# Optimization experiments

Hardware: AMD Instinct MI355X
Metric: run time of the kernel (lower is better)

Reference implementation:

```python
import jax, jax.numpy as jnp
import numpy as np
from jax import lax

EPS = 1e-5

def binarize(x):
    # sign forward, straight-through (identity) backward, matching torch .data-trick Binarize
    return x + lax.stop_gradient(jnp.sign(x) - x)

def conv2d(x, w, pad):
    return lax.conv_general_dilated(x, w, window_strides=(1, 1),
                                    padding=[(pad, pad), (pad, pad)],
                                    dimension_numbers=('NCHW', 'OIHW', 'NCHW'))

def maxpool_k2s1(x):
    return lax.reduce_window(x, -jnp.inf, lax.max, (1, 1, 2, 2), (1, 1, 1, 1), 'VALID')

def batchnorm(x, g, b):
    # training-mode BN: batch statistics over (N, H, W)
    mean = jnp.mean(x, axis=(0, 2, 3), keepdims=True)
    var = jnp.var(x, axis=(0, 2, 3), keepdims=True)
    return (x - mean) * lax.rsqrt(var + EPS) * g[None, :, None, None] + b[None, :, None, None]

def hardtanh(x):
    return jnp.clip(x, -1.0, 1.0)

def setup_inputs() -> dict:
    key = jax.random.key(0)
    ks = jax.random.split(key, 11)
    B = 4096
    return {
        'x':   jax.random.normal(ks[0], (B, 12, 12, 15), jnp.float32),
        'w1':  jax.random.normal(ks[1], (48, 12, 3, 3), jnp.float32) * 0.1,
        'g1':  1.0 + 0.1 * jax.random.normal(ks[2], (48,), jnp.float32),
        'b1':  0.1 * jax.random.normal(ks[3], (48,), jnp.float32),
        'w2':  jax.random.normal(ks[4], (48, 48, 3, 3), jnp.float32) * 0.1,
        'g2':  1.0 + 0.1 * jax.random.normal(ks[5], (48,), jnp.float32),
        'b2':  0.1 * jax.random.normal(ks[6], (48,), jnp.float32),
        'w3':  jax.random.normal(ks[7], (48, 48, 3, 3), jnp.float32) * 0.1,
        'g3':  1.0 + 0.1 * jax.random.normal(ks[8], (48,), jnp.float32),
        'b3':  0.1 * jax.random.normal(ks[9], (48,), jnp.float32),
        'wfc': jax.random.normal(ks[10], (5, 54 * 48), jnp.float32) * 0.02,
    }

def reference(x, w1, g1, b1, w2, g2, b2, w3, g3, b3, wfc):
    # BinarizeConv2d binarizes activations (in_channels != 3) and weights; returns binarized input too
    xb1 = binarize(x)                                  # [B,12,12,15]
    h = conv2d(xb1, binarize(w1), pad=1)               # [B,48,12,15]
    h = maxpool_k2s1(h)                                # [B,48,11,14]
    h = hardtanh(batchnorm(h, g1, b1))
    xb2 = binarize(h)
    h = conv2d(xb2, binarize(w2), pad=0)               # [B,48,9,12]
    h = hardtanh(batchnorm(h, g2, b2))
    xb3 = binarize(h)
    h = conv2d(xb3, binarize(w3), pad=0)               # [B,48,7,10]
    h = maxpool_k2s1(h)                                # [B,48,6,9] -> 54 spatial
    h = hardtanh(batchnorm(h, g3, b3))
    f = h.reshape(h.shape[0], -1)                      # [B, 2592]
    fb = binarize(f)
    out = fb @ binarize(wfc).T                         # [B, 5]  (LogSoftmax defined but never applied)
    return (out, xb1, xb2, xb3, fb)
```

## Files before the change

### kernel.cpp

```cpp
#include <hip/hip_runtime.h>
#include <stdint.h>

typedef unsigned long long u64;
typedef unsigned short u16;

#define NB 4096

#define WS_STATS 0
#define WS_CONST 18432
#define WS_W1P   20480
#define WS_W2P   24576
#define WS_W3P   28672
#define WS_WFCP  32768
#define WS_A1    40960
#define WS_P1    5111808

#define OUT_OFF 0
#define XB1_OFF 20480
#define XB2_OFF 8867840
#define XB3_OFF 39145472
#define FB_OFF  60379136

__device__ __forceinline__ float fsign(float v) {
    return (v > 0.0f) ? 1.0f : ((v < 0.0f) ? -1.0f : 0.0f);
}

__global__ __launch_bounds__(512)
void kw_pack(const float* __restrict__ w1, const float* __restrict__ w2,
             const float* __restrict__ w3, const float* __restrict__ wfc,
             u16* __restrict__ W1P, u64* __restrict__ W2P, u64* __restrict__ W3P,
             u64* __restrict__ WFCP, long long* __restrict__ stats) {
    int t = threadIdx.x;
    for (int i = t; i < 2304; i += 512) stats[i] = 0;
    if (t < 432) {
        int oc = t / 9, p = t % 9;
        u16 m1 = 0;
        for (int c = 0; c < 12; ++c)
            if (w1[oc*108 + c*9 + p] > 0.0f) m1 |= (u16)(1u << c);
        W1P[t] = m1;
        u64 m2 = 0, m3 = 0;
        for (int c = 0; c < 48; ++c) {
            if (w2[oc*432 + c*9 + p] > 0.0f) m2 |= (1ull << c);
            if (w3[oc*432 + c*9 + p] > 0.0f) m3 |= (1ull << c);
        }
        W2P[t] = m2;
        W3P[t] = m3;
    }
    if (t < 205) {
        int o = t / 41, j = t % 41;
        u64 m = 0;
        for (int l = 0; l < 64; ++l) {
            int k = j*64 + l;
            if (k < 2592 && wfc[o*2592 + k] > 0.0f) m |= (1ull << l);
        }
        WFCP[t] = m;
    }
}

__global__ __launch_bounds__(64)
void kbn(const float* __restrict__ g, const float* __restrict__ bb,
         const long long* __restrict__ st, float* __restrict__ cst, float Nf) {
    int t = threadIdx.x;
    if (t < 48) {
        long long s = 0, q = 0;
        #pragma unroll
        for (int k = 0; k < 8; ++k) { s += st[t*8 + k]; q += st[(48 + t)*8 + k]; }
        double N = (double)Nf;
        double mean = (double)s / N;
        double var  = (double)q / N - mean*mean;
        double scale = (double)g[t] / sqrt(var + 1e-5);
        cst[t]      = (float)scale;
        cst[48 + t] = (float)((double)bb[t] - mean*scale);
    }
}

__global__ __launch_bounds__(256)
void k0_binx(const float* __restrict__ x, float* __restrict__ dout,
             u16* __restrict__ A1) {
    int id = blockIdx.x*256 + threadIdx.x;
    int b = id / 45, s4 = id % 45;
    const float4* xp = (const float4*)(x + b*2160);
    float4* op = (float4*)(dout + XB1_OFF + (size_t)b*2160);
    u16 m0 = 0, m1 = 0, m2 = 0, m3 = 0;
    #pragma unroll
    for (int c = 0; c < 12; ++c) {
        float4 v = xp[c*45 + s4];
        float4 o;
        o.x = fsign(v.x); o.y = fsign(v.y); o.z = fsign(v.z); o.w = fsign(v.w);
        op[c*45 + s4] = o;
        u16 bit = (u16)(1u << c);
        if (v.x > 0.0f) m0 |= bit;
        if (v.y > 0.0f) m1 |= bit;
        if (v.z > 0.0f) m2 |= bit;
        if (v.w > 0.0f) m3 |= bit;
    }
    ushort4 mm; mm.x = m0; mm.y = m1; mm.z = m2; mm.w = m3;
    *((ushort4*)(A1 + b*180 + s4*4)) = mm;
}

__global__ __launch_bounds__(192)
void k1_conv1(const u16* __restrict__ W1, const u16* __restrict__ A1,
              int* __restrict__ P1, u64* __restrict__ stats) {
    __shared__ u16 As[180];
    __shared__ int cmap_i[2160];
    __shared__ int pl_i[1848];
    signed char* cmap = (signed char*)cmap_i;
    signed char* pl = (signed char*)pl_i;
    int t = threadIdx.x, b = blockIdx.x;
    if (t < 180) As[t] = A1[b*180 + t];
    __syncthreads();
    if (t < 180) {
        int y = t / 15, xx = t % 15;
        u16 tap[9], msk[9];
        int nv = 0;
        #pragma unroll
        for (int ky = 0; ky < 3; ++ky) {
            #pragma unroll
            for (int kx = 0; kx < 3; ++kx) {
                int yy = y + ky - 1, xc = xx + kx - 1;
                bool v = (yy >= 0 && yy < 12 && xc >= 0 && xc < 15);
                int yl = min(max(yy, 0), 11), xl = min(max(xc, 0), 14);
                tap[ky*3+kx] = As[yl*15 + xl];
                msk[ky*3+kx] = v ? (u16)0xFFFF : (u16)0;
                nv += v ? 12 : 0;
            }
        }
        #pragma unroll 4
        for (int oc = 0; oc < 48; ++oc) {
            int acc = 0;
            #pragma unroll
            for (int k = 0; k < 9; ++k)
                acc += __popc((unsigned)((u16)(tap[k] ^ W1[oc*9 + k]) & msk[k]));
            cmap[oc*180 + t] = (signed char)(nv - 2*acc);
        }
    }
    __syncthreads();
    int* gp = P1 + (size_t)b*1848;
    for (int i4 = t; i4 < 1848; i4 += 192) {
        int r = 0;
        #pragma unroll
        for (int u = 0; u < 4; ++u) {
            int i = i4*4 + u;
            int c = i / 154, s = i % 154, py = s / 14, px = s % 14;
            int base = c*180 + py*15 + px;
            int mx = max(max((int)cmap[base],    (int)cmap[base+1]),
                         max((int)cmap[base+15], (int)cmap[base+16]));
            r |= (mx & 0xff) << (8*u);
        }
        pl_i[i4] = r;
        gp[i4] = r;
    }
    __syncthreads();
    int wv = t >> 6, ln = t & 63, slot = b & 7;
    for (int c = wv; c < 48; c += 3) {
        int sum = 0, sq = 0;
        for (int s = ln; s < 154; s += 64) {
            int v = pl[c*154 + s];
            sum += v; sq += v*v;
        }
        #pragma unroll
        for (int off = 32; off >= 1; off >>= 1) {
            sum += __shfl_down(sum, off);
            sq  += __shfl_down(sq, off);
        }
        if (ln == 0) {
            atomicAdd((u64*)&stats[c*8 + slot],        (u64)(long long)sum);
            atomicAdd((u64*)&stats[(48 + c)*8 + slot], (u64)(long long)sq);
        }
    }
}

__global__ __launch_bounds__(256)
void kA_bn1conv2(const float* __restrict__ cst, const int4* __restrict__ P1,
                 float* __restrict__ dout, u64* __restrict__ A2,
                 const u64* __restrict__ W2, u64* __restrict__ stats) {
    __shared__ float sc[48], sh[48];
    __shared__ int sm_i[1848];
    __shared__ u64 As[154];
    __shared__ short c2s[5184];
    signed char* sm = (signed char*)sm_i;
    int t = threadIdx.x, b = blockIdx.x;
    const int4* gp = P1 + (size_t)b*462;
    for (int i = t; i < 462; i += 256) ((int4*)sm_i)[i] = gp[i];
    if (t < 48) sc[t] = cst[t];
    else if (t < 96) sh[t - 48] = cst[t];
    __syncthreads();
    float4* xo = (float4*)(dout + XB2_OFF + (size_t)b*7392);
    for (int i4 = t; i4 < 1848; i4 += 256) {
        int pv = sm_i[i4];
        int i = i4*4;
        float4 o;
        int c0 = i/154, c1 = (i+1)/154, c2i = (i+2)/154, c3 = (i+3)/154;
        o.x = fsign(sc[c0]*(float)(signed char)(pv)        + sh[c0]);
        o.y = fsign(sc[c1]*(float)(signed char)(pv >> 8)   + sh[c1]);
        o.z = fsign(sc[c2i]*(float)(signed char)(pv >> 16) + sh[c2i]);
        o.w = fsign(sc[c3]*(float)(signed char)(pv >> 24)  + sh[c3]);
        xo[i4] = o;
    }
    if (t < 154) {
        u64 m = 0;
        #pragma unroll
        for (int c = 0; c < 48; ++c)
            if (sc[c]*(float)sm[c*154 + t] + sh[c] > 0.0f) m |= (1ull << c);
        As[t] = m;
        A2[(size_t)b*154 + t] = m;
    }
    __syncthreads();
    if (t < 216) {
        int pos = (t < 108) ? t : (t - 108);
        int ocb = (t < 108) ? 0 : 24;
        int oy = pos / 12, ox = pos % 12;
        u64 tap[9];
        #pragma unroll
        for (int ky = 0; ky < 3; ++ky)
            #pragma unroll
            for (int kx = 0; kx < 3; ++kx)
                tap[ky*3+kx] = As[(oy+ky)*14 + ox + kx];
        #pragma unroll 4
        for (int oc = ocb; oc < ocb + 24; ++oc) {
            int acc = 0;
            #pragma unroll
            for (int k = 0; k < 9; ++k)
                acc += __popcll(tap[k] ^ W2[oc*9 + k]);
            c2s[oc*108 + pos] = (short)(432 - 2*acc);
        }
    }
    __syncthreads();
    int wv = t >> 6, ln = t & 63, slot = b & 7;
    for (int c = wv; c < 48; c += 4) {
        int sum = 0, sq = 0;
        for (int s = ln; s < 108; s += 64) {
            int v = c2s[c*108 + s];
            sum += v; sq += v*v;
        }
        #pragma unroll
        for (int off = 32; off >= 1; off >>= 1) {
            sum += __shfl_down(sum, off);
            sq  += __shfl_down(sq, off);
        }
        if (ln == 0) {
            atomicAdd((u64*)&stats[(96 + c)*8 + slot],  (u64)(long long)sum);
            atomicAdd((u64*)&stats[(144 + c)*8 + slot], (u64)(long long)sq);
        }
    }
}

__global__ __launch_bounds__(256)
void kB_bn2conv3(const float* __restrict__ cst, const u64* __restrict__ A2,
                 const u64* __restrict__ W2, const u64* __restrict__ W3,
                 float* __restrict__ dout, short* __restrict__ P3,
                 u64* __restrict__ stats) {
    __shared__ float sc[48], sh[48];
    __shared__ u64 As[154];
    __shared__ short c2s[5184];
    __shared__ u64 A3[108];
    __shared__ short cm[3360];
    __shared__ short pls[2592];
    int t = threadIdx.x, b = blockIdx.x;
    if (t < 154) As[t] = A2[(size_t)b*154 + t];
    if (t < 48) sc[t] = cst[t];
    else if (t < 96) sh[t - 48] = cst[t];
    __syncthreads();
    if (t < 216) {
        int pos = (t < 108) ? t : (t - 108);
        int ocb = (t < 108) ? 0 : 24;
        int oy = pos / 12, ox = pos % 12;
        u64 tap[9];
        #pragma unroll
        for (int ky = 0; ky < 3; ++ky)
            #pragma unroll
            for (int kx = 0; kx < 3; ++kx)
                tap[ky*3+kx] = As[(oy+ky)*14 + ox + kx];
        #pragma unroll 4
        for (int oc = ocb; oc < ocb + 24; ++oc) {
            int acc = 0;
            #pragma unroll
            for (int k = 0; k < 9; ++k)
                acc += __popcll(tap[k] ^ W2[oc*9 + k]);
            c2s[oc*108 + pos] = (short)(432 - 2*acc);
        }
    }
    __syncthreads();
    float4* xo = (float4*)(dout + XB3_OFF + (size_t)b*5184);
    for (int i4 = t; i4 < 1296; i4 += 256) {
        int c = i4 / 27, s4 = i4 % 27;
        short4 v4 = *(const short4*)&c2s[c*108 + s4*4];
        float4 o;
        o.x = fsign(sc[c]*(float)v4.x + sh[c]);
        o.y = fsign(sc[c]*(float)v4.y + sh[c]);
        o.z = fsign(sc[c]*(float)v4.z + sh[c]);
        o.w = fsign(sc[c]*(float)v4.w + sh[c]);
        xo[i4] = o;
    }
    if (t < 108) {
        u64 m = 0;
        #pragma unroll
        for (int c = 0; c < 48; ++c)
            if (sc[c]*(float)c2s[c*108 + t] + sh[c] > 0.0f) m |= (1ull << c);
        A3[t] = m;
    }
    __syncthreads();
    if (t < 210) {
        int grp = (t < 70) ? 0 : ((t < 140) ? 1 : 2);
        int pos = t - grp*70;
        int ocb = grp*16;
        int oy = pos / 10, ox = pos % 10;
        u64 tap[9];
        #pragma unroll
        for (int ky = 0; ky < 3; ++ky)
            #pragma unroll
            for (int kx = 0; kx < 3; ++kx)
                tap[ky*3+kx] = A3[(oy+ky)*12 + ox + kx];
        #pragma unroll 4
        for (int oc = ocb; oc < ocb + 16; ++oc) {
            int acc = 0;
            #pragma unroll
            for (int k = 0; k < 9; ++k)
                acc += __popcll(tap[k] ^ W3[oc*9 + k]);
            cm[oc*70 + pos] = (short)(432 - 2*acc);
        }
    }
    __syncthreads();
    int* p3g = (int*)(P3 + (size_t)b*2592);
    for (int i2 = t; i2 < 1296; i2 += 256) {
        int i = i2*2;
        int c = i / 54, s = i % 54, py = s / 9, px = s % 9;
        int base = c*70 + py*10 + px;
        int m0 = max(max((int)cm[base],    (int)cm[base+1]),
                     max((int)cm[base+10], (int)cm[base+11]));
        int m1 = max(max((int)cm[base+1],  (int)cm[base+2]),
                     max((int)cm[base+11], (int)cm[base+12]));
        if (px == 8) {
            int base2 = c*70 + (py+1)*10;
            m1 = max(max((int)cm[base2],    (int)cm[base2+1]),
                     max((int)cm[base2+10], (int)cm[base2+11]));
        }
        pls[i] = (short)m0;
        pls[i+1] = (short)m1;
        p3g[i2] = (m0 & 0xffff) | (m1 << 16);
    }
    __syncthreads();
    int wv = t >> 6, ln = t & 63, slot = b & 7;
    for (int c = wv; c < 48; c += 4) {
        int sum = 0, sq = 0;
        if (ln < 54) {
            int v = pls[c*54 + ln];
            sum = v; sq = v*v;
        }
        #pragma unroll
        for (int off = 32; off >= 1; off >>= 1) {
            sum += __shfl_down(sum, off);
            sq  += __shfl_down(sq, off);
        }
        if (ln == 0) {
            atomicAdd((u64*)&stats[(192 + c)*8 + slot], (u64)(long long)sum);
            atomicAdd((u64*)&stats[(240 + c)*8 + slot], (u64)(long long)sq);
        }
    }
}

__global__ __launch_bounds__(256)
void kC_fbfc(const float* __restrict__ cst, const short* __restrict__ P3,
             const u64* __restrict__ WFC, float* __restrict__ dout) {
    __shared__ float sc[48], sh[48];
    __shared__ short4 sm4[648];
    __shared__ unsigned char nib[648];
    __shared__ u64 fbb[41];
    short* sm = (short*)sm4;
    int t = threadIdx.x, b = blockIdx.x;
    const short4* p3 = (const short4*)(P3 + (size_t)b*2592);
    for (int i4 = t; i4 < 648; i4 += 256) sm4[i4] = p3[i4];
    if (t < 48) sc[t] = cst[t];
    else if (t < 96) sh[t - 48] = cst[t];
    __syncthreads();
    float4* fo = (float4*)(dout + FB_OFF + (size_t)b*2592);
    for (int i4 = t; i4 < 648; i4 += 256) {
        int i = i4*4;
        float4 o;
        unsigned n = 0;
        int c0 = i/54, c1 = (i+1)/54, c2 = (i+2)/54, c3 = (i+3)/54;
        float v0 = sc[c0]*(float)sm[i]   + sh[c0];
        float v1 = sc[c1]*(float)sm[i+1] + sh[c1];
        float v2 = sc[c2]*(float)sm[i+2] + sh[c2];
        float v3 = sc[c3]*(float)sm[i+3] + sh[c3];
        o.x = fsign(v0); o.y = fsign(v1); o.z = fsign(v2); o.w = fsign(v3);
        if (v0 > 0.0f) n |= 1u;
        if (v1 > 0.0f) n |= 2u;
        if (v2 > 0.0f) n |= 4u;
        if (v3 > 0.0f) n |= 8u;
        fo[i4] = o;
        nib[i4] = (unsigned char)n;
    }
    __syncthreads();
    if (t < 41) {
        u64 m = 0;
        #pragma unroll
        for (int k = 0; k < 16; ++k) {
            int j = t*16 + k;
            if (j < 648) m |= ((u64)nib[j]) << (4*k);
        }
        fbb[t] = m;
    }
    __syncthreads();
    if (t < 5) {
        const u64* Wf = WFC + t*41;
        int acc = 0;
        #pragma unroll
        for (int j = 0; j < 41; ++j) acc += __popcll(fbb[j] ^ Wf[j]);
        dout[OUT_OFF + b*5 + t] = (float)(2592 - 2*acc);
    }
}

extern "C" void kernel_launch(void* const* d_in, const int* in_sizes, int n_in,
                              void* d_out, int out_size, void* d_ws, size_t ws_size,
                              hipStream_t stream) {
    const float* x   = (const float*)d_in[0];
    const float* w1  = (const float*)d_in[1];
    const float* g1  = (const float*)d_in[2];
    const float* b1  = (const float*)d_in[3];
    const float* w2  = (const float*)d_in[4];
    const float* g2  = (const float*)d_in[5];
    const float* b2  = (const float*)d_in[6];
    const float* w3  = (const float*)d_in[7];
    const float* g3  = (const float*)d_in[8];
    const float* b3  = (const float*)d_in[9];
    const float* wfc = (const float*)d_in[10];
    float* out = (float*)d_out;
    char* ws = (char*)d_ws;

    long long* stats = (long long*)(ws + WS_STATS);
    float*     cst   = (float*)(ws + WS_CONST);
    u16*       W1P   = (u16*)(ws + WS_W1P);
    u64*       W2P   = (u64*)(ws + WS_W2P);
    u64*       W3P   = (u64*)(ws + WS_W3P);
    u64*       WFCP  = (u64*)(ws + WS_WFCP);
    u16*       A1    = (u16*)(ws + WS_A1);
    u64*       A2    = (u64*)(ws + WS_A1);
    int*       P1    = (int*)(ws + WS_P1);
    short*     P3    = (short*)(ws + WS_P1);

    hipLaunchKernelGGL(kw_pack,     dim3(1),    dim3(512), 0, stream,
                       w1, w2, w3, wfc, W1P, W2P, W3P, WFCP, stats);
    hipLaunchKernelGGL(k0_binx,     dim3(720),  dim3(256), 0, stream, x, out, A1);
    hipLaunchKernelGGL(k1_conv1,    dim3(NB),   dim3(192), 0, stream,
                       W1P, A1, P1, (u64*)stats);
    hipLaunchKernelGGL(kbn,         dim3(1),    dim3(64),  0, stream,
                       g1, b1, stats, cst, 630784.0f);
    hipLaunchKernelGGL(kA_bn1conv2, dim3(NB),   dim3(256), 0, stream,
                       cst, (const int4*)P1, out, A2, W2P, (u64*)stats);
    hipLaunchKernelGGL(kbn,         dim3(1),    dim3(64),  0, stream,
                       g2, b2, stats + 96*8, cst + 96, 442368.0f);
    hipLaunchKernelGGL(kB_bn2conv3, dim3(NB),   dim3(256), 0, stream,
                       cst + 96, A2, W2P, W3P, out, P3, (u64*)stats);
    hipLaunchKernelGGL(kbn,         dim3(1),    dim3(64),  0, stream,
                       g3, b3, stats + 192*8, cst + 192, 221184.0f);
    hipLaunchKernelGGL(kC_fbfc,     dim3(NB),   dim3(256), 0, stream,
                       cst + 192, P3, WFCP, out);
}
```

Before: 720.2 us.

## Fuse input binarization into conv1 and fold BN finalization into consumer kernels

Merges the input-binarize kernel into the conv1 kernel and removes the three single-block BN-finalize kernels. Each consumer kernel now computes the BN scale and shift from the atomic stats itself. It also packs conv1 weights two taps per 32-bit word and reworks pooling and stats: each thread handles a few rows with padded row strides, and a partial-sum reduction in shared memory replaces the wave shuffles. The intent is to cut launch count, global round trips and serialization gaps, at the cost of every block redundantly recomputing the BN constants.

```diff
diff --git a/kernel.cpp b/kernel.cpp
--- a/kernel.cpp
+++ b/kernel.cpp
@@ -2,18 +2,20 @@
 #include <stdint.h>
 
 typedef unsigned long long u64;
+typedef unsigned int u32;
 typedef unsigned short u16;
+typedef unsigned char u8;
+typedef signed char s8;
 
 #define NB 4096
 
 #define WS_STATS 0
-#define WS_CONST 18432
-#define WS_W1P   20480
+#define WS_W1Q   20480
 #define WS_W2P   24576
 #define WS_W3P   28672
 #define WS_WFCP  32768
-#define WS_A1    40960
-#define WS_P1    5111808
+#define WS_A2    40960
+#define WS_P1    5087232
 
 #define OUT_OFF 0
 #define XB1_OFF 20480
@@ -24,20 +26,36 @@
 __device__ __forceinline__ float fsign(float v) {
     return (v > 0.0f) ? 1.0f : ((v < 0.0f) ? -1.0f : 0.0f);
 }
+__device__ __forceinline__ int sb8(int v, int k) {
+    return (int)(s8)(v >> (8*k));
+}
+__device__ __forceinline__ int sh16(int v, int h) {
+    return h ? (v >> 16) : (int)(short)v;
+}
 
 __global__ __launch_bounds__(512)
 void kw_pack(const float* __restrict__ w1, const float* __restrict__ w2,
              const float* __restrict__ w3, const float* __restrict__ wfc,
-             u16* __restrict__ W1P, u64* __restrict__ W2P, u64* __restrict__ W3P,
+             u32* __restrict__ W1Q, u64* __restrict__ W2P, u64* __restrict__ W3P,
              u64* __restrict__ WFCP, long long* __restrict__ stats) {
     int t = threadIdx.x;
     for (int i = t; i < 2304; i += 512) stats[i] = 0;
+    if (t < 48) {
+        u16 m1[9];
+        #pragma unroll
+        for (int p = 0; p < 9; ++p) {
+            u16 m = 0;
+            for (int c = 0; c < 12; ++c)
+                if (w1[t*108 + c*9 + p] > 0.0f) m |= (u16)(1u << c);
+            m1[p] = m;
+        }
+        #pragma unroll
+        for (int j = 0; j < 4; ++j)
+            W1Q[t*5 + j] = (u32)m1[2*j] | ((u32)m1[2*j+1] << 16);
+        W1Q[t*5 + 4] = (u32)m1[8];
+    }
     if (t < 432) {
         int oc = t / 9, p = t % 9;
-        u16 m1 = 0;
-        for (int c = 0; c < 12; ++c)
-            if (w1[oc*108 + c*9 + p] > 0.0f) m1 |= (u16)(1u << c);
-        W1P[t] = m1;
         u64 m2 = 0, m3 = 0;
         for (int c = 0; c < 48; ++c) {
             if (w2[oc*432 + c*9 + p] > 0.0f) m2 |= (1ull << c);
@@ -57,57 +75,25 @@
     }
 }
 
-__global__ __launch_bounds__(64)
-void kbn(const float* __restrict__ g, const float* __restrict__ bb,
-         const long long* __restrict__ st, float* __restrict__ cst, float Nf) {
-    int t = threadIdx.x;
-    if (t < 48) {
-        long long s = 0, q = 0;
-        #pragma unroll
-        for (int k = 0; k < 8; ++k) { s += st[t*8 + k]; q += st[(48 + t)*8 + k]; }
-        double N = (double)Nf;
-        double mean = (double)s / N;
-        double var  = (double)q / N - mean*mean;
-        double scale = (double)g[t] / sqrt(var + 1e-5);
-        cst[t]      = (float)scale;
-        cst[48 + t] = (float)((double)bb[t] - mean*scale);
-    }
-}
-
-__global__ __launch_bounds__(256)
-void k0_binx(const float* __restrict__ x, float* __restrict__ dout,
-             u16* __restrict__ A1) {
-    int id = blockIdx.x*256 + threadIdx.x;
-    int b = id / 45, s4 = id % 45;
-    const float4* xp = (const float4*)(x + b*2160);
-    float4* op = (float4*)(dout + XB1_OFF + (size_t)b*2160);
-    u16 m0 = 0, m1 = 0, m2 = 0, m3 = 0;
-    #pragma unroll
-    for (int c = 0; c < 12; ++c) {
-        float4 v = xp[c*45 + s4];
-        float4 o;
-        o.x = fsign(v.x); o.y = fsign(v.y); o.z = fsign(v.z); o.w = fsign(v.w);
-        op[c*45 + s4] = o;
-        u16 bit = (u16)(1u << c);
-        if (v.x > 0.0f) m0 |= bit;
-        if (v.y > 0.0f) m1 |= bit;
-        if (v.z > 0.0f) m2 |= bit;
-        if (v.w > 0.0f) m3 |= bit;
-    }
-    ushort4 mm; mm.x = m0; mm.y = m1; mm.z = m2; mm.w = m3;
-    *((ushort4*)(A1 + b*180 + s4*4)) = mm;
-}
-
 __global__ __launch_bounds__(192)
-void k1_conv1(const u16* __restrict__ W1, const u16* __restrict__ A1,
-              int* __restrict__ P1, u64* __restrict__ stats) {
+void k1(const float* __restrict__ x, const u32* __restrict__ W1Q,
+        float* __restrict__ dout, u8* __restrict__ P1g, u64* __restrict__ stats) {
     __shared__ u16 As[180];
-    __shared__ int cmap_i[2160];
-    __shared__ int pl_i[1848];
-    signed char* cmap = (signed char*)cmap_i;
-    signed char* pl = (signed char*)pl_i;
+    __shared__ int cmap[2304];
+    __shared__ int2 part[192];
     int t = threadIdx.x, b = blockIdx.x;
-    if (t < 180) As[t] = A1[b*180 + t];
+    if (t < 180) {
+        const float* xp = x + b*2160 + t;
+        float* xo = dout + XB1_OFF + (size_t)b*2160 + t;
+        u16 m = 0;
+        #pragma unroll
+        for (int c = 0; c < 12; ++c) {
+            float v = xp[c*180];
+            xo[c*180] = fsign(v);
+            if (v > 0.0f) m |= (u16)(1u << c);
+        }
+        As[t] = m;
+    }
     __syncthreads();
     if (t < 180) {
         int y = t / 15, xx = t % 15;
@@ -125,83 +111,118 @@
                 nv += v ? 12 : 0;
             }
         }
+        u32 tq[5], mq[5];
+        #pragma unroll
+        for (int j = 0; j < 4; ++j) {
+            tq[j] = (u32)tap[2*j] | ((u32)tap[2*j+1] << 16);
+            mq[j] = (u32)msk[2*j] | ((u32)msk[2*j+1] << 16);
+        }
+        tq[4] = tap[8]; mq[4] = msk[8];
+        s8* cb = (s8*)cmap;
         #pragma unroll 4
         for (int oc = 0; oc < 48; ++oc) {
             int acc = 0;
             #pragma unroll
-            for (int k = 0; k < 9; ++k)
-                acc += __popc((unsigned)((u16)(tap[k] ^ W1[oc*9 + k]) & msk[k]));
-            cmap[oc*180 + t] = (signed char)(nv - 2*acc);
-        }
-    }
-    __syncthreads();
-    int* gp = P1 + (size_t)b*1848;
-    for (int i4 = t; i4 < 1848; i4 += 192) {
-        int r = 0;
-        #pragma unroll
-        for (int u = 0; u < 4; ++u) {
-            int i = i4*4 + u;
-            int c = i / 154, s = i % 154, py = s / 14, px = s % 14;
-            int base = c*180 + py*15 + px;
-            int mx = max(max((int)cmap[base],    (int)cmap[base+1]),
-                         max((int)cmap[base+15], (int)cmap[base+16]));
-            r |= (mx & 0xff) << (8*u);
-        }
-        pl_i[i4] = r;
-        gp[i4] = r;
-    }
-    __syncthreads();
-    int wv = t >> 6, ln = t & 63, slot = b & 7;
-    for (int c = wv; c < 48; c += 3) {
+            for (int j = 0; j < 5; ++j)
+                acc += __popc((tq[j] ^ W1Q[oc*5 + j]) & mq[j]);
+            cb[oc*192 + y*16 + xx] = (s8)(nv - 2*acc);
+        }
+    }
+    __syncthreads();
+    {
+        int c = t >> 2, q = t & 3;
+        int r0 = 3*q, nr = (q < 3) ? 3 : 2;
+        int rowv[4][4];
+        #pragma unroll
+        for (int j = 0; j < 4; ++j)
+            if (j <= nr) {
+                #pragma unroll
+                for (int i = 0; i < 4; ++i)
+                    rowv[j][i] = cmap[c*48 + (r0 + j)*4 + i];
+            }
         int sum = 0, sq = 0;
-        for (int s = ln; s < 154; s += 64) {
-            int v = pl[c*154 + s];
-            sum += v; sq += v*v;
-        }
-        #pragma unroll
-        for (int off = 32; off >= 1; off >>= 1) {
-            sum += __shfl_down(sum, off);
-            sq  += __shfl_down(sq, off);
-        }
-        if (ln == 0) {
-            atomicAdd((u64*)&stats[c*8 + slot],        (u64)(long long)sum);
-            atomicAdd((u64*)&stats[(48 + c)*8 + slot], (u64)(long long)sq);
-        }
+        u8* gp = P1g + (size_t)b*8448 + c*176;
+        #pragma unroll
+        for (int pr = 0; pr < 3; ++pr) {
+            if (pr < nr) {
+                int o0 = 0, o1 = 0, o2 = 0, o3 = 0;
+                #pragma unroll
+                for (int k = 0; k < 14; ++k) {
+                    int a0 = sb8(rowv[pr][k>>2], k&3);
+                    int a1 = sb8(rowv[pr][(k+1)>>2], (k+1)&3);
+                    int b0 = sb8(rowv[pr+1][k>>2], k&3);
+                    int b1 = sb8(rowv[pr+1][(k+1)>>2], (k+1)&3);
+                    int mx = max(max(a0, a1), max(b0, b1));
+                    sum += mx; sq += mx*mx;
+                    int sh = 8*(k&3);
+                    if ((k>>2) == 0) o0 |= (mx & 255) << sh;
+                    else if ((k>>2) == 1) o1 |= (mx & 255) << sh;
+                    else if ((k>>2) == 2) o2 |= (mx & 255) << sh;
+                    else o3 |= (mx & 255) << sh;
+                }
+                *((int4*)(gp + (r0 + pr)*16)) = make_int4(o0, o1, o2, o3);
+            }
+        }
+        part[t] = make_int2(sum, sq);
+    }
+    __syncthreads();
+    if (t < 48) {
+        int s = 0, q = 0;
+        #pragma unroll
+        for (int k = 0; k < 4; ++k) { s += part[t*4+k].x; q += part[t*4+k].y; }
+        int slot = b & 7;
+        atomicAdd(&stats[t*8 + slot],        (u64)(long long)s);
+        atomicAdd(&stats[(48 + t)*8 + slot], (u64)(long long)q);
     }
 }
 
 __global__ __launch_bounds__(256)
-void kA_bn1conv2(const float* __restrict__ cst, const int4* __restrict__ P1,
-                 float* __restrict__ dout, u64* __restrict__ A2,
-                 const u64* __restrict__ W2, u64* __restrict__ stats) {
+void kA(const float* __restrict__ g1, const float* __restrict__ b1,
+        const long long* __restrict__ statsIn, const int4* __restrict__ P1g4,
+        float* __restrict__ dout, u64* __restrict__ A2,
+        const u64* __restrict__ W2, u64* __restrict__ statsOut) {
     __shared__ float sc[48], sh[48];
-    __shared__ int sm_i[1848];
+    __shared__ int smP[2112];
     __shared__ u64 As[154];
     __shared__ short c2s[5184];
-    signed char* sm = (signed char*)sm_i;
+    __shared__ int2 part[192];
     int t = threadIdx.x, b = blockIdx.x;
-    const int4* gp = P1 + (size_t)b*462;
-    for (int i = t; i < 462; i += 256) ((int4*)sm_i)[i] = gp[i];
-    if (t < 48) sc[t] = cst[t];
-    else if (t < 96) sh[t - 48] = cst[t];
-    __syncthreads();
+    for (int i = t; i < 528; i += 256) ((int4*)smP)[i] = P1g4[(size_t)b*528 + i];
+    if (t < 48) {
+        long long s = 0, q = 0;
+        #pragma unroll
+        for (int k = 0; k < 8; ++k) { s += statsIn[t*8 + k]; q += statsIn[(48 + t)*8 + k]; }
+        double N = 630784.0;
+        double mean = (double)s / N;
+        double var  = (double)q / N - mean*mean;
+        double scale = (double)g1[t] / sqrt(var + 1e-5);
+        sc[t] = (float)scale;
+        sh[t] = (float)((double)b1[t] - mean*scale);
+    }
+    __syncthreads();
+    const s8* smb = (const s8*)smP;
     float4* xo = (float4*)(dout + XB2_OFF + (size_t)b*7392);
-    for (int i4 = t; i4 < 1848; i4 += 256) {
-        int pv = sm_i[i4];
-        int i = i4*4;
-        float4 o;
-        int c0 = i/154, c1 = (i+1)/154, c2i = (i+2)/154, c3 = (i+3)/154;
-        o.x = fsign(sc[c0]*(float)(signed char)(pv)        + sh[c0]);
-        o.y = fsign(sc[c1]*(float)(signed char)(pv >> 8)   + sh[c1]);
-        o.z = fsign(sc[c2i]*(float)(signed char)(pv >> 16) + sh[c2i]);
-        o.w = fsign(sc[c3]*(float)(signed char)(pv >> 24)  + sh[c3]);
+    for (int i4 = t; i4 < 462; i4 += 256) {
+        int i = 4*i4;
+        float r[4];
+        #pragma unroll
+        for (int k = 0; k < 4; ++k) {
+            int idx = i + k;
+            int c = idx / 154, s = idx - 154*c;
+            int row = s / 14, px = s - 14*row;
+            int v = smb[c*176 + row*16 + px];
+            r[k] = fsign(sc[c]*(float)v + sh[c]);
+        }
+        float4 o; o.x = r[0]; o.y = r[1]; o.z = r[2]; o.w = r[3];
         xo[i4] = o;
     }
     if (t < 154) {
+        int row = t / 14, px = t - 14*row;
+        int po = row*16 + px;
         u64 m = 0;
         #pragma unroll
         for (int c = 0; c < 48; ++c)
-            if (sc[c]*(float)sm[c*154 + t] + sh[c] > 0.0f) m |= (1ull << c);
+            if (sc[c]*(float)smb[c*176 + po] + sh[c] > 0.0f) m |= (1ull << c);
         As[t] = m;
         A2[(size_t)b*154 + t] = m;
     }
@@ -209,7 +230,7 @@
     if (t < 216) {
         int pos = (t < 108) ? t : (t - 108);
         int ocb = (t < 108) ? 0 : 24;
-        int oy = pos / 12, ox = pos % 12;
+        int oy = pos / 12, ox = pos - 12*oy;
         u64 tap[9];
         #pragma unroll
         for (int ky = 0; ky < 3; ++ky)
@@ -226,45 +247,58 @@
         }
     }
     __syncthreads();
-    int wv = t >> 6, ln = t & 63, slot = b & 7;
-    for (int c = wv; c < 48; c += 4) {
+    if (t < 192) {
+        int c = t >> 2, q = t & 3;
+        const int* ci = (const int*)(c2s + c*108);
         int sum = 0, sq = 0;
-        for (int s = ln; s < 108; s += 64) {
-            int v = c2s[c*108 + s];
-            sum += v; sq += v*v;
-        }
-        #pragma unroll
-        for (int off = 32; off >= 1; off >>= 1) {
-            sum += __shfl_down(sum, off);
-            sq  += __shfl_down(sq, off);
-        }
-        if (ln == 0) {
-            atomicAdd((u64*)&stats[(96 + c)*8 + slot],  (u64)(long long)sum);
-            atomicAdd((u64*)&stats[(144 + c)*8 + slot], (u64)(long long)sq);
-        }
+        for (int j = q; j < 54; j += 4) {
+            int v2 = ci[j];
+            int lo = (int)(short)v2, hi = v2 >> 16;
+            sum += lo + hi; sq += lo*lo + hi*hi;
+        }
+        part[t] = make_int2(sum, sq);
+    }
+    __syncthreads();
+    if (t < 48) {
+        int s = 0, q = 0;
+        #pragma unroll
+        for (int k = 0; k < 4; ++k) { s += part[t*4+k].x; q += part[t*4+k].y; }
+        int slot = b & 7;
+        atomicAdd(&statsOut[(96 + t)*8 + slot],  (u64)(long long)s);
+        atomicAdd(&statsOut[(144 + t)*8 + slot], (u64)(long long)q);
     }
 }
 
 __global__ __launch_bounds__(256)
-void kB_bn2conv3(const float* __restrict__ cst, const u64* __restrict__ A2,
-                 const u64* __restrict__ W2, const u64* __restrict__ W3,
-                 float* __restrict__ dout, short* __restrict__ P3,
-                 u64* __restrict__ stats) {
+void kB(const float* __restrict__ g2, const float* __restrict__ b2,
+        const long long* __restrict__ statsIn, const u64* __restrict__ A2,
+        const u64* __restrict__ W2, const u64* __restrict__ W3,
+        float* __restrict__ dout, int* __restrict__ P3i,
+        u64* __restrict__ statsOut) {
     __shared__ float sc[48], sh[48];
     __shared__ u64 As[154];
     __shared__ short c2s[5184];
     __shared__ u64 A3[108];
     __shared__ short cm[3360];
-    __shared__ short pls[2592];
+    __shared__ int2 part[192];
     int t = threadIdx.x, b = blockIdx.x;
     if (t < 154) As[t] = A2[(size_t)b*154 + t];
-    if (t < 48) sc[t] = cst[t];
-    else if (t < 96) sh[t - 48] = cst[t];
+    if (t < 48) {
+        long long s = 0, q = 0;
+        #pragma unroll
+        for (int k = 0; k < 8; ++k) { s += statsIn[(96 + t)*8 + k]; q += statsIn[(144 + t)*8 + k]; }
+        double N = 442368.0;
+        double mean = (double)s / N;
+        double var  = (double)q / N - mean*mean;
+        double scale = (double)g2[t] / sqrt(var + 1e-5);
+        sc[t] = (float)scale;
+        sh[t] = (float)((double)b2[t] - mean*scale);
+    }
     __syncthreads();
     if (t < 216) {
         int pos = (t < 108) ? t : (t - 108);
         int ocb = (t < 108) ? 0 : 24;
-        int oy = pos / 12, ox = pos % 12;
+        int oy = pos / 12, ox = pos - 12*oy;
         u64 tap[9];
         #pragma unroll
         for (int ky = 0; ky < 3; ++ky)
@@ -283,7 +317,7 @@
     __syncthreads();
     float4* xo = (float4*)(dout + XB3_OFF + (size_t)b*5184);
     for (int i4 = t; i4 < 1296; i4 += 256) {
-        int c = i4 / 27, s4 = i4 % 27;
+        int c = i4 / 27, s4 = i4 - 27*c;
         short4 v4 = *(const short4*)&c2s[c*108 + s4*4];
         float4 o;
         o.x = fsign(sc[c]*(float)v4.x + sh[c]);
@@ -304,7 +338,7 @@
         int grp = (t < 70) ? 0 : ((t < 140) ? 1 : 2);
         int pos = t - grp*70;
         int ocb = grp*16;
-        int oy = pos / 10, ox = pos % 10;
+        int oy = pos / 10, ox = pos - 10*oy;
         u64 tap[9];
         #pragma unroll
         for (int ky = 0; ky < 3; ++ky)
@@ -321,75 +355,94 @@
         }
     }
     __syncthreads();
-    int* p3g = (int*)(P3 + (size_t)b*2592);
-    for (int i2 = t; i2 < 1296; i2 += 256) {
-        int i = i2*2;
-        int c = i / 54, s = i % 54, py = s / 9, px = s % 9;
-        int base = c*70 + py*10 + px;
-        int m0 = max(max((int)cm[base],    (int)cm[base+1]),
-                     max((int)cm[base+10], (int)cm[base+11]));
-        int m1 = max(max((int)cm[base+1],  (int)cm[base+2]),
-                     max((int)cm[base+11], (int)cm[base+12]));
-        if (px == 8) {
-            int base2 = c*70 + (py+1)*10;
-            m1 = max(max((int)cm[base2],    (int)cm[base2+1]),
-                     max((int)cm[base2+10], (int)cm[base2+11]));
-        }
-        pls[i] = (short)m0;
-        pls[i+1] = (short)m1;
-        p3g[i2] = (m0 & 0xffff) | (m1 << 16);
-    }
-    __syncthreads();
-    int wv = t >> 6, ln = t & 63, slot = b & 7;
-    for (int c = wv; c < 48; c += 4) {
-        int sum = 0, sq = 0;
-        if (ln < 54) {
-            int v = pls[c*54 + ln];
-            sum = v; sq = v*v;
-        }
-        #pragma unroll
-        for (int off = 32; off >= 1; off >>= 1) {
-            sum += __shfl_down(sum, off);
-            sq  += __shfl_down(sq, off);
-        }
-        if (ln == 0) {
-            atomicAdd((u64*)&stats[(192 + c)*8 + slot], (u64)(long long)sum);
-            atomicAdd((u64*)&stats[(240 + c)*8 + slot], (u64)(long long)sq);
-        }
+    {
+        int c = t >> 2, q = t & 3;
+        if (t < 192) {
+            int pr0 = (q < 2) ? 2*q : (q + 2);
+            int npr = (q < 2) ? 2 : 1;
+            int rowv[3][5];
+            const int* cmi = (const int*)(cm + c*70);
+            #pragma unroll
+            for (int j = 0; j < 3; ++j)
+                if (j <= npr) {
+                    #pragma unroll
+                    for (int i = 0; i < 5; ++i)
+                        rowv[j][i] = cmi[(pr0 + j)*5 + i];
+                }
+            int sum = 0, sq = 0;
+            int* gp = P3i + (size_t)b*1440 + c*30;
+            #pragma unroll
+            for (int pr = 0; pr < 2; ++pr) {
+                if (pr < npr) {
+                    int o[5] = {0, 0, 0, 0, 0};
+                    #pragma unroll
+                    for (int k = 0; k < 9; ++k) {
+                        int a0 = sh16(rowv[pr][k>>1], k&1);
+                        int a1 = sh16(rowv[pr][(k+1)>>1], (k+1)&1);
+                        int b0 = sh16(rowv[pr+1][k>>1], k&1);
+                        int b1 = sh16(rowv[pr+1][(k+1)>>1], (k+1)&1);
+                        int mx = max(max(a0, a1), max(b0, b1));
+                        sum += mx; sq += mx*mx;
+                        o[k>>1] |= (mx & 0xffff) << (16*(k&1));
+                    }
+                    #pragma unroll
+                    for (int j = 0; j < 5; ++j) gp[(pr0 + pr)*5 + j] = o[j];
+                }
+            }
+            part[t] = make_int2(sum, sq);
+        }
+    }
+    __syncthreads();
+    if (t < 48) {
+        int s = 0, q = 0;
+        #pragma unroll
+        for (int k = 0; k < 4; ++k) { s += part[t*4+k].x; q += part[t*4+k].y; }
+        int slot = b & 7;
+        atomicAdd(&statsOut[(192 + t)*8 + slot], (u64)(long long)s);
+        atomicAdd(&statsOut[(240 + t)*8 + slot], (u64)(long long)q);
     }
 }
 
 __global__ __launch_bounds__(256)
-void kC_fbfc(const float* __restrict__ cst, const short* __restrict__ P3,
-             const u64* __restrict__ WFC, float* __restrict__ dout) {
+void kC(const float* __restrict__ g3, const float* __restrict__ b3,
+        const long long* __restrict__ statsIn, const int4* __restrict__ P3g4,
+        const u64* __restrict__ WFC, float* __restrict__ dout) {
     __shared__ float sc[48], sh[48];
-    __shared__ short4 sm4[648];
-    __shared__ unsigned char nib[648];
+    __shared__ int smP[1440];
+    __shared__ u8 nib[648];
     __shared__ u64 fbb[41];
-    short* sm = (short*)sm4;
     int t = threadIdx.x, b = blockIdx.x;
-    const short4* p3 = (const short4*)(P3 + (size_t)b*2592);
-    for (int i4 = t; i4 < 648; i4 += 256) sm4[i4] = p3[i4];
-    if (t < 48) sc[t] = cst[t];
-    else if (t < 96) sh[t - 48] = cst[t];
-    __syncthreads();
+    for (int i = t; i < 360; i += 256) ((int4*)smP)[i] = P3g4[(size_t)b*360 + i];
+    if (t < 48) {
+        long long s = 0, q = 0;
+        #pragma unroll
+        for (int k = 0; k < 8; ++k) { s += statsIn[(192 + t)*8 + k]; q += statsIn[(240 + t)*8 + k]; }
+        double N = 221184.0;
+        double mean = (double)s / N;
+        double var  = (double)q / N - mean*mean;
+        double scale = (double)g3[t] / sqrt(var + 1e-5);
+        sc[t] = (float)scale;
+        sh[t] = (float)((double)b3[t] - mean*scale);
+    }
+    __syncthreads();
+    const short* smS = (const short*)smP;
     float4* fo = (float4*)(dout + FB_OFF + (size_t)b*2592);
     for (int i4 = t; i4 < 648; i4 += 256) {
-        int i = i4*4;
-        float4 o;
+        int i = 4*i4;
+        float r[4];
         unsigned n = 0;
-        int c0 = i/54, c1 = (i+1)/54, c2 = (i+2)/54, c3 = (i+3)/54;
-        float v0 = sc[c0]*(float)sm[i]   + sh[c0];
-        float v1 = sc[c1]*(float)sm[i+1] + sh[c1];
-        float v2 = sc[c2]*(float)sm[i+2] + sh[c2];
-        float v3 = sc[c3]*(float)sm[i+3] + sh[c3];
-        o.x = fsign(v0); o.y = fsign(v1); o.z = fsign(v2); o.w = fsign(v3);
-        if (v0 > 0.0f) n |= 1u;
-        if (v1 > 0.0f) n |= 2u;
-        if (v2 > 0.0f) n |= 4u;
-        if (v3 > 0.0f) n |= 8u;
+        #pragma unroll
+        for (int k = 0; k < 4; ++k) {
+            int idx = i + k;
+            int c = idx / 54, s = idx - 54*c;
+            int row = s / 9, px = s - 9*row;
+            float bn = sc[c]*(float)smS[c*60 + row*10 + px] + sh[c];
+            r[k] = fsign(bn);
+            if (bn > 0.0f) n |= (1u << k);
+        }
+        float4 o; o.x = r[0]; o.y = r[1]; o.z = r[2]; o.w = r[3];
         fo[i4] = o;
-        nib[i4] = (unsigned char)n;
+        nib[i4] = (u8)n;
     }
     __syncthreads();
     if (t < 41) {
@@ -429,31 +482,22 @@
     char* ws = (char*)d_ws;
 
     long long* stats = (long long*)(ws + WS_STATS);
-    float*     cst   = (float*)(ws + WS_CONST);
-    u16*       W1P   = (u16*)(ws + WS_W1P);
+    u32*       W1Q   = (u32*)(ws + WS_W1Q);
     u64*       W2P   = (u64*)(ws + WS_W2P);
     u64*       W3P   = (u64*)(ws + WS_W3P);
     u64*       WFCP  = (u64*)(ws + WS_WFCP);
-    u16*       A1    = (u16*)(ws + WS_A1);
-    u64*       A2    = (u64*)(ws + WS_A1);
-    int*       P1    = (int*)(ws + WS_P1);
-    short*     P3    = (short*)(ws + WS_P1);
-
-    hipLaunchKernelGGL(kw_pack,     dim3(1),    dim3(512), 0, stream,
-                       w1, w2, w3, wfc, W1P, W2P, W3P, WFCP, stats);
-    hipLaunchKernelGGL(k0_binx,     dim3(720),  dim3(256), 0, stream, x, out, A1);
-    hipLaunchKernelGGL(k1_conv1,    dim3(NB),   dim3(192), 0, stream,
-                       W1P, A1, P1, (u64*)stats);
-    hipLaunchKernelGGL(kbn,         dim3(1),    dim3(64),  0, stream,
-                       g1, b1, stats, cst, 630784.0f);
-    hipLaunchKernelGGL(kA_bn1conv2, dim3(NB),   dim3(256), 0, stream,
-                       cst, (const int4*)P1, out, A2, W2P, (u64*)stats);
-    hipLaunchKernelGGL(kbn,         dim3(1),    dim3(64),  0, stream,
-                       g2, b2, stats + 96*8, cst + 96, 442368.0f);
-    hipLaunchKernelGGL(kB_bn2conv3, dim3(NB),   dim3(256), 0, stream,
-                       cst + 96, A2, W2P, W3P, out, P3, (u64*)stats);
-    hipLaunchKernelGGL(kbn,         dim3(1),    dim3(64),  0, stream,
-                       g3, b3, stats + 192*8, cst + 192, 221184.0f);
-    hipLaunchKernelGGL(kC_fbfc,     dim3(NB),   dim3(256), 0, stream,
-                       cst + 192, P3, WFCP, out);
-}
+    u64*       A2    = (u64*)(ws + WS_A2);
+    u8*        P1g   = (u8*)(ws + WS_P1);
+    int*       P3i   = (int*)(ws + WS_P1);
+
+    hipLaunchKernelGGL(kw_pack, dim3(1),  dim3(512), 0, stream,
+                       w1, w2, w3, wfc, W1Q, W2P, W3P, WFCP, stats);
+    hipLaunchKernelGGL(k1,      dim3(NB), dim3(192), 0, stream,
+                       x, W1Q, out, P1g, (u64*)stats);
+    hipLaunchKernelGGL(kA,      dim3(NB), dim3(256), 0, stream,
+                       g1, b1, stats, (const int4*)P1g, out, A2, W2P, (u64*)stats);
+    hipLaunchKernelGGL(kB,      dim3(NB), dim3(256), 0, stream,
+                       g2, b2, stats, A2, W2P, W3P, out, P3i, (u64*)stats);
+    hipLaunchKernelGGL(kC,      dim3(NB), dim3(256), 0, stream,
+                       g3, b3, stats, (const int4*)P3i, WFCP, out);
+}
```

New measurement: 618.4 us. 1.16x faster.
